# Kernel optimization log

Hardware: AMD Instinct MI355X
Metric: run time of the kernel (lower is better)

The kernel has to match this reference:

```python
import jax, jax.numpy as jnp
import numpy as np

EPS = 1e-12  # torch F.normalize default eps
COMMITMENT_COST = 0.25

def l2_normalize(v, axis=-1):
    # matches torch.nn.functional.normalize(p=2): v / max(||v||, eps)
    n = jnp.linalg.norm(v, axis=axis, keepdims=True)
    return v / jnp.maximum(n, EPS)

def setup_inputs() -> dict:
    key = jax.random.key(0)
    k1, k2 = jax.random.split(key)
    N, D, K = 262144, 64, 1024
    x = jax.random.normal(k1, (N, D), dtype=jnp.float32)
    emb_weight = jax.random.normal(k2, (K, D), dtype=jnp.float32)
    return {"x": x, "emb_weight": emb_weight}

def reference(x, emb_weight):
    # x: [N, D] latents, emb_weight: [K, D] codebook
    xn = l2_normalize(x, axis=-1)                      # F.normalize(x, dim=-1)
    wn = l2_normalize(emb_weight, axis=-1)             # normalized codebook rows
    d2 = (jnp.sum(xn * xn, axis=-1, keepdims=True)
          + jnp.sum(wn * wn, axis=1)
          - 2.0 * jnp.matmul(xn, wn.T))                # [N, K]
    encoding_indices = jnp.argmin(d2, axis=1)          # [N]
    # quantize: normalize(embeddings(idx)) == wn[idx]
    quantized = wn[encoding_indices]                   # [N, D]
    q_latent_loss = jnp.mean((quantized - jax.lax.stop_gradient(xn)) ** 2)
    e_latent_loss = jnp.mean((xn - jax.lax.stop_gradient(quantized)) ** 2)
    loss = q_latent_loss + COMMITMENT_COST * e_latent_loss
    # straight-through estimator
    quantized_st = xn + jax.lax.stop_gradient(quantized - xn)
    return quantized_st, loss, encoding_indices
```

## Files before the change

### kernel.cpp

```cpp
#include <hip/hip_runtime.h>
#include <math.h>

#define N_ROWS 262144
#define DIM 64
#define K_CODES 1024
#define NT 64
#define ROWS_PER_BLOCK 128
#define EPSF 1e-12f

typedef _Float16 f16x8 __attribute__((ext_vector_type(8)));
typedef float f32x4 __attribute__((ext_vector_type(4)));


__global__ __launch_bounds__(64) void prep_codebook(
    const float* __restrict__ w, float* __restrict__ wn,
    float* __restrict__ msw, _Float16* __restrict__ wf)
{
    int k = blockIdx.x;
    int d = threadIdx.x;
    float v = w[k * DIM + d];
    float sq = v * v;
    #pragma unroll
    for (int off = 32; off; off >>= 1) sq += __shfl_xor(sq, off, 64);
    float n = fmaxf(sqrtf(sq), EPSF);
    float o = v / n;
    wn[k * DIM + d] = o;
    float s2 = o * o;
    #pragma unroll
    for (int off = 32; off; off >>= 1) s2 += __shfl_xor(s2, off, 64);
    if (d == 0) msw[k] = -0.5f * s2;

    _Float16 hi = (_Float16)o;
    _Float16 lo = (_Float16)(o - (float)hi);
    int t = k >> 4, nn = k & 15, s = d >> 5, g = (d >> 3) & 3, i = d & 7;
    size_t base = (size_t)t * 2048 + (size_t)s * 512 + (size_t)(g * 16 + nn) * 8 + i;
    wf[base] = hi;
    wf[base + 1024] = lo;
}

#define MFMA_(A, B, C) C = __builtin_amdgcn_mfma_f32_16x16x32_f16(A, B, C, 0, 0, 0)

__global__ __launch_bounds__(256, 5) void vq_main_kernel(
    const float* __restrict__ x,
    const float* __restrict__ wn,
    const float* __restrict__ msw,
    const _Float16* __restrict__ wf,
    float* __restrict__ out_q,
    float* __restrict__ out_idx,
    float* __restrict__ partial)
{
    __shared__ _Float16 bbuf[2][2048];
    __shared__ float msw_lds[K_CODES];
    __shared__ int idx_lds[ROWS_PER_BLOCK];
    __shared__ float inv_lds[ROWS_PER_BLOCK];
    __shared__ float red[4];

    const int tid = threadIdx.x;
    const int wv = tid >> 6;
    const int lane = tid & 63;
    const int nidx = lane & 15;
    const int g = lane >> 4;
    const int block_row0 = blockIdx.x * ROWS_PER_BLOCK;

    f16x8 ah[2][2], al[2][2];
    #pragma unroll
    for (int rt = 0; rt < 2; ++rt) {
        const int arow = block_row0 + wv * 32 + rt * 16 + nidx;
        const float* xrow = x + (size_t)arow * DIM + g * 8;
        float xv[2][8];
        #pragma unroll
        for (int s = 0; s < 2; ++s) {
            float4 q0 = *(const float4*)(xrow + s * 32);
            float4 q1 = *(const float4*)(xrow + s * 32 + 4);
            xv[s][0] = q0.x; xv[s][1] = q0.y; xv[s][2] = q0.z; xv[s][3] = q0.w;
            xv[s][4] = q1.x; xv[s][5] = q1.y; xv[s][6] = q1.z; xv[s][7] = q1.w;
        }
        float ss = 0.f;
        #pragma unroll
        for (int s = 0; s < 2; ++s)
            #pragma unroll
            for (int i = 0; i < 8; ++i) ss += xv[s][i] * xv[s][i];
        ss += __shfl_xor(ss, 16, 64);
        ss += __shfl_xor(ss, 32, 64);
        float nrm = fmaxf(sqrtf(ss), EPSF);
        float inv = 1.0f / nrm;
        if (g == 0) inv_lds[wv * 32 + rt * 16 + nidx] = inv;
        #pragma unroll
        for (int s = 0; s < 2; ++s)
            #pragma unroll
            for (int i = 0; i < 8; ++i) {
                float v = xv[s][i] * inv;
                _Float16 hi = (_Float16)v;
                ah[rt][s][i] = hi;
                al[rt][s][i] = (_Float16)(v - (float)hi);
            }
    }

    *(float4*)&msw_lds[tid * 4] = *(const float4*)(msw + tid * 4);

    const _Float16* gsrc = wf + (size_t)tid * 8;
    {
        f16x8 s0 = *(const f16x8*)(gsrc);
        *(f16x8*)&bbuf[0][tid * 8] = s0;
    }
    f16x8 stg = *(const f16x8*)(gsrc + 2048);
    gsrc += 2 * 2048;
    __syncthreads();

    float best[2][4];
    int bt[2][4];
    #pragma unroll
    for (int rt = 0; rt < 2; ++rt)
        #pragma unroll
        for (int r = 0; r < 4; ++r) { best[rt][r] = -3.4e38f; bt[rt][r] = 0; }

    for (int t = 0; t < NT; ++t) {
        const int cur = t & 1;
        const _Float16* bp = &bbuf[cur][lane * 8];
        f16x8 b0 = *(const f16x8*)(bp);
        f16x8 b1 = *(const f16x8*)(bp + 512);
        f16x8 b2 = *(const f16x8*)(bp + 1024);
        f16x8 b3 = *(const f16x8*)(bp + 1536);
        float mval = msw_lds[t * 16 + nidx];

        f32x4 acc0 = {mval, mval, mval, mval};
        f32x4 acc1 = acc0;
        __builtin_amdgcn_s_setprio(1);
        MFMA_(ah[0][0], b0, acc0); MFMA_(ah[1][0], b0, acc1);
        MFMA_(ah[0][1], b1, acc0); MFMA_(ah[1][1], b1, acc1);
        MFMA_(al[0][0], b0, acc0); MFMA_(al[1][0], b0, acc1);
        MFMA_(al[0][1], b1, acc0); MFMA_(al[1][1], b1, acc1);
        MFMA_(ah[0][0], b2, acc0); MFMA_(ah[1][0], b2, acc1);
        MFMA_(ah[0][1], b3, acc0); MFMA_(ah[1][1], b3, acc1);
        __builtin_amdgcn_s_setprio(0);

        if (t + 1 < NT) {
            *(f16x8*)&bbuf[cur ^ 1][tid * 8] = stg;
            if (t + 2 < NT) {
                stg = *(const f16x8*)(gsrc);
                gsrc += 2048;
            }
        }

        #pragma unroll
        for (int r = 0; r < 4; ++r) {
            if (acc0[r] > best[0][r]) { best[0][r] = acc0[r]; bt[0][r] = t; }
            if (acc1[r] > best[1][r]) { best[1][r] = acc1[r]; bt[1][r] = t; }
        }
        __syncthreads();
    }

    #pragma unroll
    for (int rt = 0; rt < 2; ++rt)
        #pragma unroll
        for (int r = 0; r < 4; ++r) {
            float b = best[rt][r];
            int bi = bt[rt][r] * 16 + nidx;
            #pragma unroll
            for (int off = 1; off <= 8; off <<= 1) {
                float ob = __shfl_xor(b, off, 64);
                int oi = __shfl_xor(bi, off, 64);
                if (ob > b || (ob == b && oi < bi)) { b = ob; bi = oi; }
            }
            if (nidx == 0)
                idx_lds[wv * 32 + rt * 16 + g * 4 + r] = bi;
        }
    __syncthreads();

    const int lr = tid >> 1;
    const int grow = block_row0 + lr;
    const int d0 = (tid & 1) * 32;
    const int ci = idx_lds[lr];
    const float invn = inv_lds[lr];
    const float4* xp = (const float4*)(x + (size_t)grow * DIM + d0);
    const float4* qp = (const float4*)(wn + (size_t)ci * DIM + d0);
    float4* op = (float4*)(out_q + (size_t)grow * DIM + d0);
    float ls = 0.f;
    #pragma unroll
    for (int i = 0; i < 8; ++i) {
        float4 qv = qp[i];
        float4 xv4 = xp[i];
        float e0 = qv.x - xv4.x * invn;
        float e1 = qv.y - xv4.y * invn;
        float e2 = qv.z - xv4.z * invn;
        float e3 = qv.w - xv4.w * invn;
        ls += e0 * e0 + e1 * e1 + e2 * e2 + e3 * e3;
        op[i] = qv;
    }
    if (!(tid & 1)) out_idx[grow] = (float)ci;

    float s = ls;
    #pragma unroll
    for (int off = 32; off; off >>= 1) s += __shfl_xor(s, off, 64);
    if (lane == 0) red[wv] = s;
    __syncthreads();
    if (tid == 0) partial[blockIdx.x] = (red[0] + red[1]) + (red[2] + red[3]);
}

__global__ __launch_bounds__(256) void finalize_kernel(
    const float* __restrict__ partial, float* __restrict__ loss_out)
{
    __shared__ float red[4];
    int t = threadIdx.x;
    float s = 0.f;
    #pragma unroll
    for (int i = 0; i < 8; ++i) s += partial[t * 8 + i];
    #pragma unroll
    for (int off = 32; off; off >>= 1) s += __shfl_xor(s, off, 64);
    if ((t & 63) == 0) red[t >> 6] = s;
    __syncthreads();
    if (t == 0)
        *loss_out = 1.25f * (((red[0] + red[1]) + (red[2] + red[3]))
                             / (float)((size_t)N_ROWS * DIM));
}

extern "C" void kernel_launch(void* const* d_in, const int* in_sizes, int n_in,
                              void* d_out, int out_size, void* d_ws, size_t ws_size,
                              hipStream_t stream) {
    const float* x = (const float*)d_in[0];
    const float* w = (const float*)d_in[1];
    float* out = (float*)d_out;
    float* ws = (float*)d_ws;

    float* wn      = ws;
    float* msw     = wn + (size_t)K_CODES * DIM;
    float* partial = msw + K_CODES;
    _Float16* wf   = (_Float16*)(partial + 2048);

    float* out_q    = out;
    float* out_loss = out + (size_t)N_ROWS * DIM;
    float* out_idx  = out_loss + 1;

    prep_codebook<<<K_CODES, 64, 0, stream>>>(w, wn, msw, wf);
    vq_main_kernel<<<N_ROWS / ROWS_PER_BLOCK, 256, 0, stream>>>(
        x, wn, msw, wf, out_q, out_idx, partial);
    finalize_kernel<<<1, 256, 0, stream>>>(partial, out_loss);
}
```

Measured before the change: 120.2 us.

## Use single fp16 distance pass with margin-based exact fixup for ambiguous rows

The main kernel now computes distances with a single fp16 hi-term MFMA pass instead of the three-term split-precision scheme. It also tracks the top-2 scores per row and appends rows whose margin falls under a threshold to a global list via an atomic counter. A new fixup kernel recomputes those rows with the full split-precision MFMA. Where the argmin changes, it rewrites the quantized output and index and adds a loss correction. This cuts MFMA work and LDS traffic for most rows, at the cost of extra kernels, atomics and correctness that depends on the margin bound.

```diff
diff --git a/kernel.cpp b/kernel.cpp
--- a/kernel.cpp
+++ b/kernel.cpp
@@ -7,10 +7,16 @@
 #define NT 64
 #define ROWS_PER_BLOCK 128
 #define EPSF 1e-12f
+#define MARGIN 2.0e-3f
 
 typedef _Float16 f16x8 __attribute__((ext_vector_type(8)));
+typedef _Float16 f16x4 __attribute__((ext_vector_type(4)));
 typedef float f32x4 __attribute__((ext_vector_type(4)));
 
+
+__global__ void init_kernel(int* counter) {
+    if (threadIdx.x == 0) *counter = 0;
+}
 
 __global__ __launch_bounds__(64) void prep_codebook(
     const float* __restrict__ w, float* __restrict__ wn,
@@ -47,9 +53,11 @@
     const _Float16* __restrict__ wf,
     float* __restrict__ out_q,
     float* __restrict__ out_idx,
-    float* __restrict__ partial)
+    float* __restrict__ partial,
+    int* __restrict__ counter,
+    int* __restrict__ list)
 {
-    __shared__ _Float16 bbuf[2][2048];
+    __shared__ _Float16 bbuf[2][1024];
     __shared__ float msw_lds[K_CODES];
     __shared__ int idx_lds[ROWS_PER_BLOCK];
     __shared__ float inv_lds[ROWS_PER_BLOCK];
@@ -62,7 +70,7 @@
     const int g = lane >> 4;
     const int block_row0 = blockIdx.x * ROWS_PER_BLOCK;
 
-    f16x8 ah[2][2], al[2][2];
+    f16x8 ah[2][2];
     #pragma unroll
     for (int rt = 0; rt < 2; ++rt) {
         const int arow = block_row0 + wv * 32 + rt * 16 + nidx;
@@ -88,64 +96,57 @@
         #pragma unroll
         for (int s = 0; s < 2; ++s)
             #pragma unroll
-            for (int i = 0; i < 8; ++i) {
-                float v = xv[s][i] * inv;
-                _Float16 hi = (_Float16)v;
-                ah[rt][s][i] = hi;
-                al[rt][s][i] = (_Float16)(v - (float)hi);
-            }
+            for (int i = 0; i < 8; ++i)
+                ah[rt][s][i] = (_Float16)(xv[s][i] * inv);
     }
 
     *(float4*)&msw_lds[tid * 4] = *(const float4*)(msw + tid * 4);
 
-    const _Float16* gsrc = wf + (size_t)tid * 8;
+    const _Float16* gsrc = wf + (size_t)tid * 4;
     {
-        f16x8 s0 = *(const f16x8*)(gsrc);
-        *(f16x8*)&bbuf[0][tid * 8] = s0;
+        f16x4 s0 = *(const f16x4*)(gsrc);
+        *(f16x4*)&bbuf[0][tid * 4] = s0;
     }
-    f16x8 stg = *(const f16x8*)(gsrc + 2048);
+    f16x4 stg = *(const f16x4*)(gsrc + 2048);
     gsrc += 2 * 2048;
     __syncthreads();
 
-    float best[2][4];
-    int bt[2][4];
+    float b1v[2][4], b2v[2][4];
+    int bti[2][4];
     #pragma unroll
     for (int rt = 0; rt < 2; ++rt)
         #pragma unroll
-        for (int r = 0; r < 4; ++r) { best[rt][r] = -3.4e38f; bt[rt][r] = 0; }
+        for (int r = 0; r < 4; ++r) {
+            b1v[rt][r] = -3.4e38f; b2v[rt][r] = -3.4e38f; bti[rt][r] = 0;
+        }
 
     for (int t = 0; t < NT; ++t) {
         const int cur = t & 1;
         const _Float16* bp = &bbuf[cur][lane * 8];
         f16x8 b0 = *(const f16x8*)(bp);
         f16x8 b1 = *(const f16x8*)(bp + 512);
-        f16x8 b2 = *(const f16x8*)(bp + 1024);
-        f16x8 b3 = *(const f16x8*)(bp + 1536);
         float mval = msw_lds[t * 16 + nidx];
 
         f32x4 acc0 = {mval, mval, mval, mval};
         f32x4 acc1 = acc0;
-        __builtin_amdgcn_s_setprio(1);
         MFMA_(ah[0][0], b0, acc0); MFMA_(ah[1][0], b0, acc1);
         MFMA_(ah[0][1], b1, acc0); MFMA_(ah[1][1], b1, acc1);
-        MFMA_(al[0][0], b0, acc0); MFMA_(al[1][0], b0, acc1);
-        MFMA_(al[0][1], b1, acc0); MFMA_(al[1][1], b1, acc1);
-        MFMA_(ah[0][0], b2, acc0); MFMA_(ah[1][0], b2, acc1);
-        MFMA_(ah[0][1], b3, acc0); MFMA_(ah[1][1], b3, acc1);
-        __builtin_amdgcn_s_setprio(0);
 
         if (t + 1 < NT) {
-            *(f16x8*)&bbuf[cur ^ 1][tid * 8] = stg;
+            *(f16x4*)&bbuf[cur ^ 1][tid * 4] = stg;
             if (t + 2 < NT) {
-                stg = *(const f16x8*)(gsrc);
+                stg = *(const f16x4*)(gsrc);
                 gsrc += 2048;
             }
         }
 
         #pragma unroll
         for (int r = 0; r < 4; ++r) {
-            if (acc0[r] > best[0][r]) { best[0][r] = acc0[r]; bt[0][r] = t; }
-            if (acc1[r] > best[1][r]) { best[1][r] = acc1[r]; bt[1][r] = t; }
+            float s0 = acc0[r], s1 = acc1[r];
+            b2v[0][r] = fmaxf(b2v[0][r], fminf(s0, b1v[0][r]));
+            if (s0 > b1v[0][r]) { b1v[0][r] = s0; bti[0][r] = t; }
+            b2v[1][r] = fmaxf(b2v[1][r], fminf(s1, b1v[1][r]));
+            if (s1 > b1v[1][r]) { b1v[1][r] = s1; bti[1][r] = t; }
         }
         __syncthreads();
     }
@@ -154,16 +155,25 @@
     for (int rt = 0; rt < 2; ++rt)
         #pragma unroll
         for (int r = 0; r < 4; ++r) {
-            float b = best[rt][r];
-            int bi = bt[rt][r] * 16 + nidx;
+            float b1 = b1v[rt][r], b2 = b2v[rt][r];
+            int i1 = bti[rt][r] * 16 + nidx;
             #pragma unroll
             for (int off = 1; off <= 8; off <<= 1) {
-                float ob = __shfl_xor(b, off, 64);
-                int oi = __shfl_xor(bi, off, 64);
-                if (ob > b || (ob == b && oi < bi)) { b = ob; bi = oi; }
-            }
-            if (nidx == 0)
-                idx_lds[wv * 32 + rt * 16 + g * 4 + r] = bi;
+                float ob1 = __shfl_xor(b1, off, 64);
+                int   oi1 = __shfl_xor(i1, off, 64);
+                float ob2 = __shfl_xor(b2, off, 64);
+                float loser = fminf(b1, ob1);
+                b2 = fmaxf(fmaxf(b2, ob2), loser);
+                if (ob1 > b1 || (ob1 == b1 && oi1 < i1)) { b1 = ob1; i1 = oi1; }
+            }
+            if (nidx == 0) {
+                const int lrow = wv * 32 + rt * 16 + g * 4 + r;
+                idx_lds[lrow] = i1;
+                if (b1 - b2 <= MARGIN) {
+                    int pos = atomicAdd(counter, 1);
+                    list[pos] = block_row0 + lrow;
+                }
+            }
         }
     __syncthreads();
 
@@ -197,14 +207,179 @@
     if (tid == 0) partial[blockIdx.x] = (red[0] + red[1]) + (red[2] + red[3]);
 }
 
+__global__ __launch_bounds__(256, 4) void fixup_kernel(
+    const float* __restrict__ x,
+    const float* __restrict__ wn,
+    const float* __restrict__ msw,
+    const _Float16* __restrict__ wf,
+    const int* __restrict__ counter,
+    const int* __restrict__ list,
+    float* __restrict__ out_q,
+    float* __restrict__ out_idx,
+    float* __restrict__ partial2)
+{
+    __shared__ int rows_lds[128];
+    __shared__ int idx_lds[128];
+    __shared__ float inv_lds[128];
+    __shared__ float red[4];
+
+    const int tid = threadIdx.x;
+    const int wv = tid >> 6;
+    const int lane = tid & 63;
+    const int nidx = lane & 15;
+    const int g = lane >> 4;
+    const int cnt = *counter;
+    float dsum = 0.f;
+
+    for (int b = blockIdx.x; b * 128 < cnt; b += gridDim.x) {
+        const int rbase = b * 128;
+        const int nrows = min(128, cnt - rbase);
+        __syncthreads();
+        if (tid < 128) rows_lds[tid] = list[rbase + min(tid, nrows - 1)];
+        __syncthreads();
+
+        f16x8 ah[2][2], al[2][2];
+        #pragma unroll
+        for (int rt = 0; rt < 2; ++rt) {
+            const int lr0 = wv * 32 + rt * 16 + nidx;
+            const int arow = rows_lds[lr0];
+            const float* xrow = x + (size_t)arow * DIM + g * 8;
+            float xv[2][8];
+            #pragma unroll
+            for (int s = 0; s < 2; ++s) {
+                float4 q0 = *(const float4*)(xrow + s * 32);
+                float4 q1 = *(const float4*)(xrow + s * 32 + 4);
+                xv[s][0] = q0.x; xv[s][1] = q0.y; xv[s][2] = q0.z; xv[s][3] = q0.w;
+                xv[s][4] = q1.x; xv[s][5] = q1.y; xv[s][6] = q1.z; xv[s][7] = q1.w;
+            }
+            float ss = 0.f;
+            #pragma unroll
+            for (int s = 0; s < 2; ++s)
+                #pragma unroll
+                for (int i = 0; i < 8; ++i) ss += xv[s][i] * xv[s][i];
+            ss += __shfl_xor(ss, 16, 64);
+            ss += __shfl_xor(ss, 32, 64);
+            float nrm = fmaxf(sqrtf(ss), EPSF);
+            float inv = 1.0f / nrm;
+            if (g == 0) inv_lds[lr0] = inv;
+            #pragma unroll
+            for (int s = 0; s < 2; ++s)
+                #pragma unroll
+                for (int i = 0; i < 8; ++i) {
+                    float v = xv[s][i] * inv;
+                    _Float16 hi = (_Float16)v;
+                    ah[rt][s][i] = hi;
+                    al[rt][s][i] = (_Float16)(v - (float)hi);
+                }
+        }
+
+        const _Float16* bbase = wf + (size_t)lane * 8;
+        f16x8 cb0 = *(const f16x8*)(bbase);
+        f16x8 cb1 = *(const f16x8*)(bbase + 512);
+        f16x8 cb2 = *(const f16x8*)(bbase + 1024);
+        f16x8 cb3 = *(const f16x8*)(bbase + 1536);
+        float mval = msw[nidx];
+
+        float best[2][4];
+        int bt[2][4];
+        #pragma unroll
+        for (int rt = 0; rt < 2; ++rt)
+            #pragma unroll
+            for (int r = 0; r < 4; ++r) { best[rt][r] = -3.4e38f; bt[rt][r] = 0; }
+
+        for (int t = 0; t < NT; ++t) {
+            const _Float16* np = bbase + (size_t)(t + 1) * 2048;
+            f16x8 nb0 = *(const f16x8*)(np);
+            f16x8 nb1 = *(const f16x8*)(np + 512);
+            f16x8 nb2 = *(const f16x8*)(np + 1024);
+            f16x8 nb3 = *(const f16x8*)(np + 1536);
+            float nmval = (t + 1 < NT) ? msw[(t + 1) * 16 + nidx] : 0.f;
+
+            f32x4 acc0 = {mval, mval, mval, mval};
+            f32x4 acc1 = acc0;
+            MFMA_(ah[0][0], cb0, acc0); MFMA_(ah[1][0], cb0, acc1);
+            MFMA_(ah[0][1], cb1, acc0); MFMA_(ah[1][1], cb1, acc1);
+            MFMA_(al[0][0], cb0, acc0); MFMA_(al[1][0], cb0, acc1);
+            MFMA_(al[0][1], cb1, acc0); MFMA_(al[1][1], cb1, acc1);
+            MFMA_(ah[0][0], cb2, acc0); MFMA_(ah[1][0], cb2, acc1);
+            MFMA_(ah[0][1], cb3, acc0); MFMA_(ah[1][1], cb3, acc1);
+
+            #pragma unroll
+            for (int r = 0; r < 4; ++r) {
+                if (acc0[r] > best[0][r]) { best[0][r] = acc0[r]; bt[0][r] = t; }
+                if (acc1[r] > best[1][r]) { best[1][r] = acc1[r]; bt[1][r] = t; }
+            }
+            cb0 = nb0; cb1 = nb1; cb2 = nb2; cb3 = nb3; mval = nmval;
+        }
+
+        #pragma unroll
+        for (int rt = 0; rt < 2; ++rt)
+            #pragma unroll
+            for (int r = 0; r < 4; ++r) {
+                float bb = best[rt][r];
+                int bi = bt[rt][r] * 16 + nidx;
+                #pragma unroll
+                for (int off = 1; off <= 8; off <<= 1) {
+                    float ob = __shfl_xor(bb, off, 64);
+                    int oi = __shfl_xor(bi, off, 64);
+                    if (ob > bb || (ob == bb && oi < bi)) { bb = ob; bi = oi; }
+                }
+                if (nidx == 0)
+                    idx_lds[wv * 32 + rt * 16 + g * 4 + r] = bi;
+            }
+        __syncthreads();
+
+        const int lr = tid >> 1;
+        if (lr < nrows) {
+            const int row = rows_lds[lr];
+            const int cn = idx_lds[lr];
+            const int co = (int)out_idx[row];
+            if (cn != co) {
+                const int d0 = (tid & 1) * 32;
+                const float invn = inv_lds[lr];
+                const float4* xp = (const float4*)(x + (size_t)row * DIM + d0);
+                const float4* qn = (const float4*)(wn + (size_t)cn * DIM + d0);
+                const float4* qo = (const float4*)(wn + (size_t)co * DIM + d0);
+                float4* op = (float4*)(out_q + (size_t)row * DIM + d0);
+                #pragma unroll
+                for (int i = 0; i < 8; ++i) {
+                    float4 xv4 = xp[i];
+                    float4 qnv = qn[i];
+                    float4 qov = qo[i];
+                    float xn0 = xv4.x * invn, xn1 = xv4.y * invn;
+                    float xn2 = xv4.z * invn, xn3 = xv4.w * invn;
+                    float a0 = qnv.x - xn0, a1 = qnv.y - xn1,
+                          a2 = qnv.z - xn2, a3 = qnv.w - xn3;
+                    float c0 = qov.x - xn0, c1 = qov.y - xn1,
+                          c2 = qov.z - xn2, c3 = qov.w - xn3;
+                    dsum += (a0 * a0 + a1 * a1 + a2 * a2 + a3 * a3)
+                          - (c0 * c0 + c1 * c1 + c2 * c2 + c3 * c3);
+                    op[i] = qnv;
+                }
+                if (!(tid & 1)) out_idx[row] = (float)cn;
+            }
+        }
+        __syncthreads();
+    }
+
+    float s = dsum;
+    #pragma unroll
+    for (int off = 32; off; off >>= 1) s += __shfl_xor(s, off, 64);
+    if (lane == 0) red[wv] = s;
+    __syncthreads();
+    if (tid == 0) partial2[blockIdx.x] = (red[0] + red[1]) + (red[2] + red[3]);
+}
+
 __global__ __launch_bounds__(256) void finalize_kernel(
-    const float* __restrict__ partial, float* __restrict__ loss_out)
+    const float* __restrict__ partial, const float* __restrict__ partial2,
+    float* __restrict__ loss_out)
 {
     __shared__ float red[4];
     int t = threadIdx.x;
     float s = 0.f;
     #pragma unroll
     for (int i = 0; i < 8; ++i) s += partial[t * 8 + i];
+    s += partial2[t];
     #pragma unroll
     for (int off = 32; off; off >>= 1) s += __shfl_xor(s, off, 64);
     if ((t & 63) == 0) red[t >> 6] = s;
@@ -222,17 +397,23 @@
     float* out = (float*)d_out;
     float* ws = (float*)d_ws;
 
-    float* wn      = ws;
-    float* msw     = wn + (size_t)K_CODES * DIM;
-    float* partial = msw + K_CODES;
-    _Float16* wf   = (_Float16*)(partial + 2048);
+    float* wn       = ws;
+    float* msw      = wn + (size_t)K_CODES * DIM;
+    float* partial  = msw + K_CODES;
+    float* partial2 = partial + 2048;
+    int*   counter  = (int*)(partial2 + 256);
+    int*   list     = counter + 1;
+    _Float16* wf    = (_Float16*)(ws + 331012);
 
     float* out_q    = out;
     float* out_loss = out + (size_t)N_ROWS * DIM;
     float* out_idx  = out_loss + 1;
 
+    init_kernel<<<1, 64, 0, stream>>>(counter);
     prep_codebook<<<K_CODES, 64, 0, stream>>>(w, wn, msw, wf);
     vq_main_kernel<<<N_ROWS / ROWS_PER_BLOCK, 256, 0, stream>>>(
-        x, wn, msw, wf, out_q, out_idx, partial);
-    finalize_kernel<<<1, 256, 0, stream>>>(partial, out_loss);
-}
+        x, wn, msw, wf, out_q, out_idx, partial, counter, list);
+    fixup_kernel<<<256, 256, 0, stream>>>(
+        x, wn, msw, wf, counter, list, out_q, out_idx, partial2);
+    finalize_kernel<<<1, 256, 0, stream>>>(partial, partial2, out_loss);
+}
```

New measurement: 247.5 us. 106% more time.
